# Performance work log

Hardware: AMD Instinct MI355X
Metric: run time of the kernel (lower is better)

## Reference

```python
import jax, jax.numpy as jnp
import numpy as np
import math

B, S, H, A = 128, 2048, 512, 512

def setup_inputs() -> dict:
    key = jax.random.key(0)
    k1, k2, k3 = jax.random.split(key, 3)
    return {
        "lstm_output": jax.random.normal(k1, (B, S, H), dtype=jnp.float32),
        "w_omega": jax.random.normal(k2, (H, A), dtype=jnp.float32) * (1.0 / math.sqrt(2 * H)),
        "b_omega": jnp.zeros((A,), dtype=jnp.float32),
        "u_omega": jax.random.normal(k3, (A,), dtype=jnp.float32) * (1.0 / math.sqrt(A)),
    }

def reference(lstm_output, w_omega, b_omega, u_omega):
    # v: [B, S, A] = tanh(x @ W + b) / sqrt(A)
    scale = math.sqrt(w_omega.shape[1])
    v = jnp.tanh(jnp.einsum('bsh,ha->bsa', lstm_output, w_omega) + b_omega) / scale
    vu = jnp.einsum('bsa,a->bs', v, u_omega)  # [B, S]
    max_vu = jnp.max(vu, axis=1, keepdims=True)
    exp_vu = jnp.exp(vu - max_vu)
    alphas = exp_vu / (jnp.sum(exp_vu, axis=1, keepdims=True) + 1e-10)  # [B, S]
    output = jnp.einsum('bs,bsh->bh', alphas, lstm_output)  # [B, H]
    return (output, alphas)
```

## Files before the change

kernel.cpp:

```cpp
#include <hip/hip_runtime.h>
#include <hip/hip_bf16.h>
#include <math.h>


#define M_TOK 262144
#define HDIM 512
#define ADIM 512
#define SDIM 2048
#define BDIM 128

typedef __attribute__((ext_vector_type(8))) short short8;
typedef __attribute__((ext_vector_type(4))) float f32x4;

static __device__ __forceinline__ unsigned short f2bf(float f) {
    unsigned u = __builtin_bit_cast(unsigned, f);
    unsigned rnd = 0x7FFFu + ((u >> 16) & 1u);
    return (unsigned short)((u + rnd) >> 16);
}

__global__ void k_wswz(const float* __restrict__ W, unsigned short* __restrict__ Wswz) {
    int t = blockIdx.x * 256 + threadIdx.x;
    int lane = t & 63;
    int frag = t >> 6;
    int kb = frag >> 5;
    int nb = frag & 31;
    int n  = nb * 16 + (lane & 15);
    int k0 = kb * 32 + (lane >> 4) * 8;
    short8 s;
#pragma unroll
    for (int j = 0; j < 8; ++j)
        s[j] = (short)f2bf(W[(k0 + j) * ADIM + n]);
    reinterpret_cast<short8*>(Wswz)[t] = s;
}

__global__ __launch_bounds__(256, 2)
void k_gemm_vu(const float* __restrict__ X, const unsigned short* __restrict__ Wswz,
               const float* __restrict__ bvec, const float* __restrict__ u,
               float* __restrict__ vu) {
    __shared__ __align__(16) unsigned short Xs[64][520];
    __shared__ float vured[4][64];

    const int tid  = threadIdx.x;
    const int lane = tid & 63;
    const int wave = tid >> 6;
    const int lm   = lane & 15;
    const int quad = lane >> 4;
    const int r0   = blockIdx.x * 64;

    const float4* Xp = reinterpret_cast<const float4*>(X + (size_t)r0 * HDIM);
#pragma unroll 8
    for (int it = 0; it < 32; ++it) {
        int idx  = it * 256 + tid;
        int row  = idx >> 7;
        int col4 = idx & 127;
        float4 v = Xp[idx];
        unsigned lo = (unsigned)f2bf(v.x) | ((unsigned)f2bf(v.y) << 16);
        unsigned hi = (unsigned)f2bf(v.z) | ((unsigned)f2bf(v.w) << 16);
        unsigned* d = reinterpret_cast<unsigned*>(&Xs[row][col4 * 4]);
        d[0] = lo; d[1] = hi;
    }
    __syncthreads();

    const short8* wbl = reinterpret_cast<const short8*>(Wswz) + lane + wave * 512;

    f32x4 acc[4][8];
#pragma unroll
    for (int i = 0; i < 4; ++i)
#pragma unroll
        for (int j = 0; j < 8; ++j)
            acc[i][j] = (f32x4){0.f, 0.f, 0.f, 0.f};

    short8 bcur[8], bnxt[8];
#pragma unroll
    for (int j = 0; j < 8; ++j) bcur[j] = wbl[j * 64];

    for (int kb = 0; kb < 16; ++kb) {
        if (kb < 15) {
#pragma unroll
            for (int j = 0; j < 8; ++j) bnxt[j] = wbl[(kb + 1) * 2048 + j * 64];
        }
        short8 a[4];
#pragma unroll
        for (int i = 0; i < 4; ++i)
            a[i] = *reinterpret_cast<const short8*>(&Xs[i * 16 + lm][kb * 32 + quad * 8]);
#pragma unroll
        for (int i = 0; i < 4; ++i)
#pragma unroll
            for (int j = 0; j < 8; ++j)
                acc[i][j] = __builtin_amdgcn_mfma_f32_16x16x32_bf16(a[i], bcur[j], acc[i][j], 0, 0, 0);
#pragma unroll
        for (int j = 0; j < 8; ++j) bcur[j] = bnxt[j];
    }

    float vus[16];
#pragma unroll
    for (int q = 0; q < 16; ++q) vus[q] = 0.f;
    const int colbase = wave * 128 + lm;
#pragma unroll
    for (int j = 0; j < 8; ++j) {
        int col  = colbase + j * 16;
        float uu = u[col];
        float bb = bvec[col];
#pragma unroll
        for (int i = 0; i < 4; ++i)
#pragma unroll
            for (int r = 0; r < 4; ++r) {
                float x = acc[i][j][r] + bb;
                float e = __expf(2.0f * x);
                float t = 1.0f - 2.0f / (e + 1.0f);
                vus[i * 4 + r] += t * uu;
            }
    }
#pragma unroll
    for (int m = 1; m <= 8; m <<= 1) {
#pragma unroll
        for (int q = 0; q < 16; ++q)
            vus[q] += __shfl_xor(vus[q], m, 64);
    }
    if (lm == 0) {
#pragma unroll
        for (int i = 0; i < 4; ++i)
#pragma unroll
            for (int r = 0; r < 4; ++r)
                vured[wave][i * 16 + quad * 4 + r] = vus[i * 4 + r];
    }
    __syncthreads();
    if (tid < 64) {
        float s = vured[0][tid] + vured[1][tid] + vured[2][tid] + vured[3][tid];
        vu[r0 + tid] = s * 0.044194173824159216f;
    }
}

__global__ void k_softmax(float* __restrict__ out) {
    float* vu = out + 65536 + (size_t)blockIdx.x * SDIM;
    const int tid  = threadIdx.x;
    const int lane = tid & 63;
    const int wave = tid >> 6;
    __shared__ float red[8];

    float v[8];
#pragma unroll
    for (int i = 0; i < 8; ++i) v[i] = vu[tid + 256 * i];

    float mx = v[0];
#pragma unroll
    for (int i = 1; i < 8; ++i) mx = fmaxf(mx, v[i]);
#pragma unroll
    for (int m = 1; m <= 32; m <<= 1) mx = fmaxf(mx, __shfl_xor(mx, m, 64));
    if (lane == 0) red[wave] = mx;
    __syncthreads();
    mx = fmaxf(fmaxf(red[0], red[1]), fmaxf(red[2], red[3]));

    float e[8], s = 0.f;
#pragma unroll
    for (int i = 0; i < 8; ++i) { e[i] = __expf(v[i] - mx); s += e[i]; }
#pragma unroll
    for (int m = 1; m <= 32; m <<= 1) s += __shfl_xor(s, m, 64);
    if (lane == 0) red[4 + wave] = s;
    __syncthreads();
    s = red[4] + red[5] + red[6] + red[7];

    float invs = 1.0f / (s + 1e-10f);
#pragma unroll
    for (int i = 0; i < 8; ++i) vu[tid + 256 * i] = e[i] * invs;
}

__global__ __launch_bounds__(256)
void k_wsum(const float* __restrict__ X, float* __restrict__ out) {
    const int blk = blockIdx.x;
    const int b   = blk >> 3;
    const int sc  = blk & 7;
    const float* alp = out + 65536 + (size_t)b * SDIM + sc * 256;
    const float* xb  = X + ((size_t)b * SDIM + sc * 256) * HDIM;
    const int tid = threadIdx.x;
    float a0 = 0.f, a1 = 0.f;
#pragma unroll 4
    for (int s = 0; s < 256; ++s) {
        float al = alp[s];
        a0 = fmaf(al, xb[(size_t)s * HDIM + tid], a0);
        a1 = fmaf(al, xb[(size_t)s * HDIM + tid + 256], a1);
    }
    atomicAdd(&out[b * HDIM + tid], a0);
    atomicAdd(&out[b * HDIM + tid + 256], a1);
}

extern "C" void kernel_launch(void* const* d_in, const int* in_sizes, int n_in,
                              void* d_out, int out_size, void* d_ws, size_t ws_size,
                              hipStream_t stream) {
    const float* X  = (const float*)d_in[0];
    const float* W  = (const float*)d_in[1];
    const float* bb = (const float*)d_in[2];
    const float* u  = (const float*)d_in[3];
    float* out = (float*)d_out;
    unsigned short* Wswz = (unsigned short*)d_ws;

    k_wswz<<<128, 256, 0, stream>>>(W, Wswz);
    k_gemm_vu<<<M_TOK / 64, 256, 0, stream>>>(X, Wswz, bb, u, out + 65536);
    k_softmax<<<BDIM, 256, 0, stream>>>(out);
    hipMemsetAsync(d_out, 0, 65536 * sizeof(float), stream);
    k_wsum<<<BDIM * 8, 256, 0, stream>>>(X, out);
}
```

Measured before the change: 861.0 us.

## Fuse weighted sum into GEMM with split-softmax partials and combine kernel

```diff
diff --git a/kernel.cpp b/kernel.cpp
--- a/kernel.cpp
+++ b/kernel.cpp
@@ -8,6 +8,10 @@
 #define ADIM 512
 #define SDIM 2048
 #define BDIM 128
+
+#define WSWZ_FLOATS 131072
+#define PART_STRIDE 514
+#define NCHUNK 4096
 
 typedef __attribute__((ext_vector_type(8))) short short8;
 typedef __attribute__((ext_vector_type(4))) float f32x4;
@@ -34,11 +38,12 @@
 }
 
 __global__ __launch_bounds__(256, 2)
-void k_gemm_vu(const float* __restrict__ X, const unsigned short* __restrict__ Wswz,
-               const float* __restrict__ bvec, const float* __restrict__ u,
-               float* __restrict__ vu) {
+void k_gemm_fused(const float* __restrict__ X, const unsigned short* __restrict__ Wswz,
+                  const float* __restrict__ bvec, const float* __restrict__ u,
+                  float* __restrict__ vu, float* __restrict__ part) {
     __shared__ __align__(16) unsigned short Xs[64][520];
     __shared__ float vured[4][64];
+    __shared__ float e_lds[64];
 
     const int tid  = threadIdx.x;
     const int lane = tid & 63;
@@ -46,6 +51,7 @@
     const int lm   = lane & 15;
     const int quad = lane >> 4;
     const int r0   = blockIdx.x * 64;
+    float* pblk    = part + (size_t)blockIdx.x * PART_STRIDE;
 
     const float4* Xp = reinterpret_cast<const float4*>(X + (size_t)r0 * HDIM);
 #pragma unroll 8
@@ -125,63 +131,81 @@
                 vured[wave][i * 16 + quad * 4 + r] = vus[i * 4 + r];
     }
     __syncthreads();
+
     if (tid < 64) {
-        float s = vured[0][tid] + vured[1][tid] + vured[2][tid] + vured[3][tid];
-        vu[r0 + tid] = s * 0.044194173824159216f;
-    }
-}
-
-__global__ void k_softmax(float* __restrict__ out) {
-    float* vu = out + 65536 + (size_t)blockIdx.x * SDIM;
-    const int tid  = threadIdx.x;
-    const int lane = tid & 63;
-    const int wave = tid >> 6;
-    __shared__ float red[8];
-
-    float v[8];
-#pragma unroll
-    for (int i = 0; i < 8; ++i) v[i] = vu[tid + 256 * i];
-
-    float mx = v[0];
-#pragma unroll
-    for (int i = 1; i < 8; ++i) mx = fmaxf(mx, v[i]);
-#pragma unroll
-    for (int m = 1; m <= 32; m <<= 1) mx = fmaxf(mx, __shfl_xor(mx, m, 64));
-    if (lane == 0) red[wave] = mx;
-    __syncthreads();
-    mx = fmaxf(fmaxf(red[0], red[1]), fmaxf(red[2], red[3]));
-
-    float e[8], s = 0.f;
-#pragma unroll
-    for (int i = 0; i < 8; ++i) { e[i] = __expf(v[i] - mx); s += e[i]; }
-#pragma unroll
-    for (int m = 1; m <= 32; m <<= 1) s += __shfl_xor(s, m, 64);
-    if (lane == 0) red[4 + wave] = s;
-    __syncthreads();
-    s = red[4] + red[5] + red[6] + red[7];
-
-    float invs = 1.0f / (s + 1e-10f);
-#pragma unroll
-    for (int i = 0; i < 8; ++i) vu[tid + 256 * i] = e[i] * invs;
+        float v = (vured[0][tid] + vured[1][tid] + vured[2][tid] + vured[3][tid])
+                  * 0.044194173824159216f;
+        vu[r0 + tid] = v;
+        float m = v;
+#pragma unroll
+        for (int j = 1; j <= 32; j <<= 1) m = fmaxf(m, __shfl_xor(m, j, 64));
+        float e = __expf(v - m);
+        e_lds[tid] = e;
+        float l = e;
+#pragma unroll
+        for (int j = 1; j <= 32; j <<= 1) l += __shfl_xor(l, j, 64);
+        if (tid == 0) { pblk[512] = m; pblk[513] = l; }
+    }
+    __syncthreads();
+
+    float o0 = 0.f, o1 = 0.f;
+    const int c2 = tid * 2;
+#pragma unroll 8
+    for (int s = 0; s < 64; ++s) {
+        unsigned uu = *reinterpret_cast<const unsigned*>(&Xs[s][c2]);
+        float e  = e_lds[s];
+        float xl = __builtin_bit_cast(float, uu << 16);
+        float xh = __builtin_bit_cast(float, uu & 0xFFFF0000u);
+        o0 = fmaf(e, xl, o0);
+        o1 = fmaf(e, xh, o1);
+    }
+    *reinterpret_cast<float2*>(&pblk[c2]) = make_float2(o0, o1);
 }
 
 __global__ __launch_bounds__(256)
-void k_wsum(const float* __restrict__ X, float* __restrict__ out) {
-    const int blk = blockIdx.x;
-    const int b   = blk >> 3;
-    const int sc  = blk & 7;
-    const float* alp = out + 65536 + (size_t)b * SDIM + sc * 256;
-    const float* xb  = X + ((size_t)b * SDIM + sc * 256) * HDIM;
-    const int tid = threadIdx.x;
-    float a0 = 0.f, a1 = 0.f;
-#pragma unroll 4
-    for (int s = 0; s < 256; ++s) {
-        float al = alp[s];
-        a0 = fmaf(al, xb[(size_t)s * HDIM + tid], a0);
-        a1 = fmaf(al, xb[(size_t)s * HDIM + tid + 256], a1);
-    }
-    atomicAdd(&out[b * HDIM + tid], a0);
-    atomicAdd(&out[b * HDIM + tid + 256], a1);
+void k_combine(const float* __restrict__ part, float* __restrict__ out,
+               float* __restrict__ params) {
+    const int b = blockIdx.x, tid = threadIdx.x;
+    __shared__ float wch[32];
+    __shared__ float sinv;
+    const float* pb = part + (size_t)b * 32 * PART_STRIDE;
+    if (tid < 32) {
+        float m = pb[tid * PART_STRIDE + 512];
+        float l = pb[tid * PART_STRIDE + 513];
+        float M = m;
+#pragma unroll
+        for (int j = 1; j <= 16; j <<= 1) M = fmaxf(M, __shfl_xor(M, j, 32));
+        float w  = __expf(m - M);
+        float lw = l * w;
+#pragma unroll
+        for (int j = 1; j <= 16; j <<= 1) lw += __shfl_xor(lw, j, 32);
+        wch[tid] = w;
+        if (tid == 0) {
+            float inv = 1.0f / (lw + 1e-10f);
+            sinv = inv;
+            params[b] = M;
+            params[BDIM + b] = inv;
+        }
+    }
+    __syncthreads();
+    float inv = sinv;
+    float o0 = 0.f, o1 = 0.f;
+    const int h = tid * 2;
+#pragma unroll 8
+    for (int c = 0; c < 32; ++c) {
+        float w = wch[c];
+        float2 v = *reinterpret_cast<const float2*>(&pb[c * PART_STRIDE + h]);
+        o0 = fmaf(w, v.x, o0);
+        o1 = fmaf(w, v.y, o1);
+    }
+    out[b * HDIM + h]     = o0 * inv;
+    out[b * HDIM + h + 1] = o1 * inv;
+}
+
+__global__ void k_alphas(float* __restrict__ vu, const float* __restrict__ params) {
+    int i = blockIdx.x * 256 + threadIdx.x;
+    int b = i >> 11;
+    vu[i] = __expf(vu[i] - params[b]) * params[BDIM + b];
 }
 
 extern "C" void kernel_launch(void* const* d_in, const int* in_sizes, int n_in,
@@ -192,11 +216,13 @@
     const float* bb = (const float*)d_in[2];
     const float* u  = (const float*)d_in[3];
     float* out = (float*)d_out;
+
     unsigned short* Wswz = (unsigned short*)d_ws;
+    float* part   = (float*)d_ws + WSWZ_FLOATS;
+    float* params = (float*)d_ws + WSWZ_FLOATS + NCHUNK * PART_STRIDE;
 
     k_wswz<<<128, 256, 0, stream>>>(W, Wswz);
-    k_gemm_vu<<<M_TOK / 64, 256, 0, stream>>>(X, Wswz, bb, u, out + 65536);
-    k_softmax<<<BDIM, 256, 0, stream>>>(out);
-    hipMemsetAsync(d_out, 0, 65536 * sizeof(float), stream);
-    k_wsum<<<BDIM * 8, 256, 0, stream>>>(X, out);
-}
+    k_gemm_fused<<<NCHUNK, 256, 0, stream>>>(X, Wswz, bb, u, out + 65536, part);
+    k_combine<<<BDIM, 256, 0, stream>>>(part, out, params);
+    k_alphas<<<M_TOK / 256, 256, 0, stream>>>(out + 65536, params);
+}
```

After: 798.1 us. -7.3%, faster.
